# Kernel tuning notes

Measured on AMD Instinct MI355X. Metric: run time of the kernel, lower is better.

The kernel has to match this reference:

```python
import jax, jax.numpy as jnp
import numpy as np

COMMIT_LAMBDA = 0.25


def setup_inputs() -> dict:
    key = jax.random.key(0)
    k1, k2 = jax.random.split(key)
    B, C, T = 8, 256, 1024
    NCB, K, D = 2, 8192, 128
    x = jax.random.normal(k1, (B, C, T), dtype=jnp.float32)
    # EMA codebook weights buffer (init: randn * 0.1)
    codebooks = jax.random.normal(k2, (NCB, K, D), dtype=jnp.float32) * 0.1
    return {"x": x, "codebooks": codebooks}


def reference(x, codebooks):
    B, C, T = x.shape
    ncb, K, d = codebooks.shape
    # [B, C, T] -> [B*T, ncb, d]
    xs = x.reshape(B, ncb, d, T).transpose(0, 3, 1, 2).reshape(B * T, ncb, d)
    # squared euclidean distances (argmin-equivalent to cdist)
    x2 = jnp.sum(xs * xs, axis=-1)[..., None]            # [N, ncb, 1]
    c2 = jnp.sum(codebooks * codebooks, axis=-1)[None]    # [1, ncb, K]
    xc = jnp.einsum('bnd,nkd->bnk', xs, codebooks)        # [N, ncb, K]
    d2 = x2 - 2.0 * xc + c2
    idx = jnp.argmin(d2, axis=-1)                         # [N, ncb] int
    # gather nearest code vectors: [N, ncb, d]
    q = codebooks[jnp.arange(ncb)[None, :], idx]
    # straight-through estimator
    q_st = xs + jax.lax.stop_gradient(q - xs)
    # commitment loss (training mode): sum over codebooks of mse(x_i, q_i.detach())
    loss = COMMIT_LAMBDA * jnp.sum(
        jnp.mean((xs - jax.lax.stop_gradient(q)) ** 2, axis=(0, 2))
    )
    # reassemble to [B, C, T]
    quantized = q_st.reshape(B, T, ncb, d).transpose(0, 2, 3, 1).reshape(B, C, T)
    indices = idx.reshape(B, T, ncb).transpose(0, 2, 1)   # [B, ncb, T]
    return quantized, indices, loss
```

## Files before the change

### kernel.cpp

```cpp
#include <hip/hip_runtime.h>
#include <hip/hip_bf16.h>

#define BB   8
#define TT   1024
#define NCBN 2
#define DD   128
#define KK   8192
#define MM   8192

constexpr int OUT_IDX_OFF  = BB * 256 * TT;
constexpr int OUT_LOSS_OFF = OUT_IDX_OFF + BB * NCBN * TT;

#define THR   0.45f
#define QCAP  768

typedef __attribute__((ext_vector_type(8))) short   short8;
typedef __attribute__((ext_vector_type(4))) float   float4v;

__device__ __forceinline__ unsigned short f2bf(float v) {
    unsigned u = __float_as_uint(v);
    return (unsigned short)((u + 0x7FFFu + ((u >> 16) & 1u)) >> 16);
}

__device__ __forceinline__ void gl_lds16(const void* g, void* l) {
    __builtin_amdgcn_global_load_lds(
        (const __attribute__((address_space(1))) unsigned int*)g,
        (__attribute__((address_space(3))) unsigned int*)l, 16, 0, 0);
}

__global__ __launch_bounds__(256)
void pack_x_kernel(const float* __restrict__ x, unsigned short* __restrict__ xbf,
                   float* __restrict__ x2, unsigned long long* __restrict__ pmin) {
    __shared__ float Ld[DD][65];
    const int b = blockIdx.x >> 1, n = blockIdx.x & 1;
    const int t0 = blockIdx.y * 64;
    const int tid = threadIdx.x;

    const float* base = x + ((size_t)(b * 256 + n * 128)) * TT + t0;
    const int dro = tid >> 2, q4 = tid & 3;
#pragma unroll
    for (int half = 0; half < 2; ++half) {
        int d = dro + half * 64;
        const float* rp = base + (size_t)d * TT + q4 * 16;
#pragma unroll
        for (int j = 0; j < 4; ++j) {
            float4 v = *(const float4*)(rp + j * 4);
            int t = q4 * 16 + j * 4;
            Ld[d][t + 0] = v.x; Ld[d][t + 1] = v.y;
            Ld[d][t + 2] = v.z; Ld[d][t + 3] = v.w;
        }
    }
    __syncthreads();

    if (tid < 64) {
        float s = 0.f;
        for (int d = 0; d < DD; ++d) { float v = Ld[d][tid]; s = fmaf(v, v, s); }
        x2[(size_t)n * MM + b * TT + t0 + tid] = s;
        pmin[(size_t)n * MM + b * TT + t0 + tid] = 0xFFFFFFFFFFFFFFFFull;
    }

    unsigned short* orow0 = xbf + ((size_t)n * MM + b * TT + t0) * DD;
#pragma unroll
    for (int pp = 0; pp < 4; ++pp) {
        int u = tid + pp * 256;
        int tt = u >> 4, sg = u & 15;
        unsigned short tmp[8];
#pragma unroll
        for (int j = 0; j < 8; ++j) tmp[j] = f2bf(Ld[sg * 8 + j][tt]);
        uint4 pk;
        pk.x = (unsigned)tmp[0] | ((unsigned)tmp[1] << 16);
        pk.y = (unsigned)tmp[2] | ((unsigned)tmp[3] << 16);
        pk.z = (unsigned)tmp[4] | ((unsigned)tmp[5] << 16);
        pk.w = (unsigned)tmp[6] | ((unsigned)tmp[7] << 16);
        *(uint4*)(orow0 + (size_t)tt * DD + sg * 8) = pk;
    }
}

__global__ __launch_bounds__(256)
void pack_c_kernel(const float* __restrict__ cb, unsigned short* __restrict__ cbf,
                   float* __restrict__ c2, float* __restrict__ out) {
    int g = blockIdx.x * 256 + threadIdx.x;
    if (g == 0) out[OUT_LOSS_OFF] = 0.f;
    const float4* crow = (const float4*)(cb + (size_t)g * DD);
    unsigned short* orow = cbf + (size_t)g * DD;
    float s = 0.f;
#pragma unroll 4
    for (int i2 = 0; i2 < 16; ++i2) {
        float4 v0 = crow[2 * i2];
        float4 v1 = crow[2 * i2 + 1];
        s = fmaf(v0.x, v0.x, s); s = fmaf(v0.y, v0.y, s);
        s = fmaf(v0.z, v0.z, s); s = fmaf(v0.w, v0.w, s);
        s = fmaf(v1.x, v1.x, s); s = fmaf(v1.y, v1.y, s);
        s = fmaf(v1.z, v1.z, s); s = fmaf(v1.w, v1.w, s);
        uint4 pk;
        pk.x = (unsigned)f2bf(v0.x) | ((unsigned)f2bf(v0.y) << 16);
        pk.y = (unsigned)f2bf(v0.z) | ((unsigned)f2bf(v0.w) << 16);
        pk.z = (unsigned)f2bf(v1.x) | ((unsigned)f2bf(v1.y) << 16);
        pk.w = (unsigned)f2bf(v1.z) | ((unsigned)f2bf(v1.w) << 16);
        *(uint4*)(orow + i2 * 8) = pk;
    }
    c2[g] = s;
}

__device__ void rescore_one(int n, int m, int k,
                            const float* __restrict__ x, const float* __restrict__ cb,
                            const float* __restrict__ x2, const float* __restrict__ c2,
                            unsigned long long* __restrict__ pmin) {
    int b = m >> 10, t = m & (TT - 1);
    const float* xp = x + ((size_t)(b * 256 + n * 128)) * TT + t;
    const float* cp = cb + ((size_t)(n * KK + k)) * DD;
    float xc = 0.f;
    for (int d = 0; d < DD; ++d)
        xc = fmaf(xp[(size_t)d * TT], cp[d], xc);
    float u = x2[n * MM + m] - 2.0f * xc;
    float s = u + c2[n * KK + k];
    unsigned long long pk = ((unsigned long long)__float_as_uint(s) << 32) | (unsigned)k;
    atomicMin(pmin + (size_t)n * MM + m, pk);
}

__global__ __launch_bounds__(256, 2)
void screen_kernel(const unsigned short* __restrict__ xbf,
                   const unsigned short* __restrict__ cbf,
                   const float* __restrict__ c2,
                   const float* __restrict__ x,
                   const float* __restrict__ cb32,
                   const float* __restrict__ x2,
                   unsigned long long* __restrict__ pmin) {
    __shared__ __align__(16) unsigned short Qsh[128 * 128];
    __shared__ __align__(16) unsigned short Ash[128 * 128];
    __shared__ unsigned int   minU[128];
    __shared__ float          c2s[128];
    __shared__ unsigned int   qcnt;
    __shared__ unsigned int   queue[QCAP];

    const int tid = threadIdx.x;
    const int id  = blockIdx.x;
    const int n   = id & 1;
    const int ks  = (id >> 1) & 3;
    const int qt  = id >> 3;
    const int m0  = qt * 128;
    const int k0  = ks * 2048;

    const int wave = tid >> 6, lane = tid & 63;
    const int cw = wave & 1, qw = wave >> 1;
    const int quad = lane >> 4, l15 = lane & 15;

    int goff[8];
#pragma unroll
    for (int p = 0; p < 8; ++p) {
        int u   = (p * 4 + wave) * 64 + lane;
        int row = u >> 4;
        int seg = (u & 15) ^ (row & 15);
        goff[p] = (row * DD + seg * 8) * 2;
    }

    {
        const char* src = (const char*)(xbf + ((size_t)n * MM + m0) * DD);
#pragma unroll
        for (int p = 0; p < 8; ++p)
            gl_lds16(src + goff[p], &Qsh[(p * 4 + wave) * 512]);
    }
    if (tid < 128) minU[tid] = 0xFFFFFFFFu;
    if (tid == 0)  qcnt = 0;
    __syncthreads();

    short8 bfr[4][4];
#pragma unroll
    for (int tq = 0; tq < 4; ++tq) {
        int q = qw * 64 + tq * 16 + l15;
#pragma unroll
        for (int k4 = 0; k4 < 4; ++k4) {
            int seg = k4 * 4 + quad;
            bfr[tq][k4] = *(const short8*)(&Qsh[q * 128 + ((seg ^ l15) * 8)]);
        }
    }

    float mloc[4] = {3.4e38f, 3.4e38f, 3.4e38f, 3.4e38f};
    float thr[4]  = {3.4e38f, 3.4e38f, 3.4e38f, 3.4e38f};

    const char*  asrc0 = (const char*)(cbf + ((size_t)n * KK + k0) * DD);
    const float* c2p   = c2 + (size_t)n * KK + k0;

#pragma unroll
    for (int phase = 0; phase < 2; ++phase) {
        for (int ch = 0; ch < 16; ++ch) {
            __syncthreads();
            {
                const char* src = asrc0 + (size_t)ch * (128 * DD * 2);
#pragma unroll
                for (int p = 0; p < 8; ++p)
                    gl_lds16(src + goff[p], &Ash[(p * 4 + wave) * 512]);
                if (tid < 32)
                    *(float4*)&c2s[tid * 4] =
                        *(const float4*)(c2p + ch * 128 + tid * 4);
            }
            __syncthreads();

            float4v acc[4][4];
#pragma unroll
            for (int tc = 0; tc < 4; ++tc)
#pragma unroll
                for (int tq = 0; tq < 4; ++tq)
                    acc[tc][tq] = (float4v){0.f, 0.f, 0.f, 0.f};

#pragma unroll
            for (int k4 = 0; k4 < 4; ++k4) {
                short8 a[4];
#pragma unroll
                for (int tc = 0; tc < 4; ++tc) {
                    int r = cw * 64 + tc * 16 + l15;
                    int seg = k4 * 4 + quad;
                    a[tc] = *(const short8*)(&Ash[r * 128 + ((seg ^ l15) * 8)]);
                }
#pragma unroll
                for (int tc = 0; tc < 4; ++tc)
#pragma unroll
                    for (int tq = 0; tq < 4; ++tq)
                        acc[tc][tq] = __builtin_amdgcn_mfma_f32_16x16x32_bf16(
                            a[tc], bfr[tq][k4], acc[tc][tq], 0, 0, 0);
            }

#pragma unroll
            for (int tc = 0; tc < 4; ++tc) {
                float4v c2r = *(const float4v*)(&c2s[cw * 64 + tc * 16 + quad * 4]);
#pragma unroll
                for (int tq = 0; tq < 4; ++tq) {
                    float y0 = fmaf(-2.0f, acc[tc][tq][0], c2r[0]);
                    float y1 = fmaf(-2.0f, acc[tc][tq][1], c2r[1]);
                    float y2 = fmaf(-2.0f, acc[tc][tq][2], c2r[2]);
                    float y3 = fmaf(-2.0f, acc[tc][tq][3], c2r[3]);
                    float m4 = fminf(fminf(y0, y1), fminf(y2, y3));
                    if (phase == 0) {
                        mloc[tq] = fminf(mloc[tq], m4);
                    } else if (m4 <= thr[tq]) {
                        float yv[4] = {y0, y1, y2, y3};
#pragma unroll
                        for (int rg = 0; rg < 4; ++rg) {
                            if (yv[rg] <= thr[tq]) {
                                unsigned idx  = atomicAdd(&qcnt, 1u);
                                unsigned code = (unsigned)(ch * 128 + cw * 64 + tc * 16 + quad * 4 + rg);
                                unsigned q    = (unsigned)(qw * 64 + tq * 16 + l15);
                                if (idx < QCAP) queue[idx] = (q << 11) | code;
                                else rescore_one(n, m0 + (int)q, k0 + (int)code,
                                                 x, cb32, x2, c2, pmin);
                            }
                        }
                    }
                }
            }
        }

        if (phase == 0) {
#pragma unroll
            for (int tq = 0; tq < 4; ++tq) {
                float v = mloc[tq];
                v = fminf(v, __shfl_xor(v, 16, 64));
                v = fminf(v, __shfl_xor(v, 32, 64));
                if (quad == 0) {
                    unsigned u  = __float_as_uint(v);
                    unsigned mu = (u & 0x80000000u) ? ~u : (u | 0x80000000u);
                    atomicMin(&minU[qw * 64 + tq * 16 + l15], mu);
                }
            }
            __syncthreads();
#pragma unroll
            for (int tq = 0; tq < 4; ++tq) {
                unsigned mu = minU[qw * 64 + tq * 16 + l15];
                unsigned u  = (mu & 0x80000000u) ? (mu & 0x7FFFFFFFu) : ~mu;
                thr[tq] = __uint_as_float(u) + THR;
            }
        }
    }

    __syncthreads();
    unsigned total = qcnt; if (total > QCAP) total = QCAP;
    for (unsigned i = tid; i < total; i += 256) {
        unsigned ent = queue[i];
        rescore_one(n, m0 + (int)(ent >> 11), k0 + (int)(ent & 2047u),
                    x, cb32, x2, c2, pmin);
    }
}

__global__ __launch_bounds__(256)
void gather_kernel(const float* __restrict__ x, const float* __restrict__ cb,
                   const unsigned long long* __restrict__ pmin,
                   float* __restrict__ out) {
    __shared__ float Cr[64][DD + 1];
    __shared__ int   kid[64];
    const int b = blockIdx.x >> 1, n = blockIdx.x & 1;
    const int t0 = blockIdx.y * 64;
    const int tid = threadIdx.x;

    if (tid < 64) {
        int t = t0 + tid;
        int k = (int)(pmin[(size_t)n * MM + b * TT + t] & 0xFFFFFFFFull);
        kid[tid] = k;
        out[OUT_IDX_OFF + (b * NCBN + n) * TT + t] = (float)k;
    }
    __syncthreads();

    {
        int row = tid >> 2, q4 = tid & 3;
        const float* cp = cb + ((size_t)n * KK + kid[row]) * DD + q4 * 32;
#pragma unroll
        for (int j = 0; j < 8; ++j) {
            float4 v = *(const float4*)(cp + j * 4);
            int d = q4 * 32 + j * 4;
            Cr[row][d + 0] = v.x; Cr[row][d + 1] = v.y;
            Cr[row][d + 2] = v.z; Cr[row][d + 3] = v.w;
        }
    }
    __syncthreads();

    float lsum = 0.f;
    const float* xb = x  + ((size_t)(b * 256 + n * 128)) * TT + t0;
    float*       ob = out + ((size_t)(b * 256 + n * 128)) * TT + t0;
#pragma unroll
    for (int pp = 0; pp < 8; ++pp) {
        int u  = tid + pp * 256;
        int d  = u >> 4, ts = (u & 15) * 4;
        float4 xv = *(const float4*)(xb + (size_t)d * TT + ts);
        float4 qv = { Cr[ts + 0][d], Cr[ts + 1][d], Cr[ts + 2][d], Cr[ts + 3][d] };
        *(float4*)(ob + (size_t)d * TT + ts) = qv;
        float e;
        e = xv.x - qv.x; lsum = fmaf(e, e, lsum);
        e = xv.y - qv.y; lsum = fmaf(e, e, lsum);
        e = xv.z - qv.z; lsum = fmaf(e, e, lsum);
        e = xv.w - qv.w; lsum = fmaf(e, e, lsum);
    }

#pragma unroll
    for (int o = 32; o > 0; o >>= 1) lsum += __shfl_down(lsum, o, 64);
    __shared__ float wsum[4];
    int lane = tid & 63, w = tid >> 6;
    if (lane == 0) wsum[w] = lsum;
    __syncthreads();
    if (tid == 0) {
        float tot = wsum[0] + wsum[1] + wsum[2] + wsum[3];
        atomicAdd(out + OUT_LOSS_OFF, tot * 2.384185791015625e-7f);
    }
}

extern "C" void kernel_launch(void* const* d_in, const int* in_sizes, int n_in,
                              void* d_out, int out_size, void* d_ws, size_t ws_size,
                              hipStream_t stream) {
    (void)in_sizes; (void)n_in; (void)out_size; (void)ws_size;
    const float* x  = (const float*)d_in[0];
    const float* cb = (const float*)d_in[1];
    float* out = (float*)d_out;

    char* ws = (char*)d_ws;
    unsigned short* xbf = (unsigned short*)(ws);
    unsigned short* cbf = (unsigned short*)(ws + (4u << 20));
    float* x2 = (float*)(ws + (8u << 20));
    float* c2 = (float*)(ws + (8u << 20) + (64u << 10));
    unsigned long long* pmin =
        (unsigned long long*)(ws + (8u << 20) + (128u << 10));

    pack_x_kernel<<<dim3(16, 16), 256, 0, stream>>>(x, xbf, x2, pmin);
    pack_c_kernel<<<dim3(64), 256, 0, stream>>>(cb, cbf, c2, out);

    screen_kernel<<<dim3(512), 256, 0, stream>>>(xbf, cbf, c2, x, cb, x2, pmin);
    gather_kernel<<<dim3(16, 16), 256, 0, stream>>>(x, cb, pmin, out);
}
```

Before: 184.8 us.

## Split codebook screening 8-way with global min filter and contiguous fp32 rescore

Merges the x and codebook pack kernels into one launch and splits the K dimension into 8 slices. This doubles screen blocks to 1024, and a shared LDS buffer replaces the separate Q and A tiles to cut LDS use. Each block publishes its phase-0 row minima to a global atomic array. Queued candidates now store their approximate score, so the final rescore skips entries above the cross-slice threshold. A transposed fp32 copy of x, written when workspace allows, makes rescore reads contiguous. Risks include reading a partially updated global minimum, which is still safe but filters less, and extra writes of the fp32 copy.

Result: slower. 196.7 us (+6.4%).

```diff
diff --git a/kernel.cpp b/kernel.cpp
--- a/kernel.cpp
+++ b/kernel.cpp
@@ -12,7 +12,8 @@
 constexpr int OUT_LOSS_OFF = OUT_IDX_OFF + BB * NCBN * TT;
 
 #define THR   0.45f
-#define QCAP  768
+#define QCAP  512
+#define NSPL  8
 
 typedef __attribute__((ext_vector_type(8))) short   short8;
 typedef __attribute__((ext_vector_type(4))) float   float4v;
@@ -28,13 +29,54 @@
         (__attribute__((address_space(3))) unsigned int*)l, 16, 0, 0);
 }
 
+__device__ __forceinline__ unsigned fmono(float v) {
+    unsigned u = __float_as_uint(v);
+    return (u & 0x80000000u) ? ~u : (u | 0x80000000u);
+}
+__device__ __forceinline__ float fmono_inv(unsigned mu) {
+    unsigned u = (mu & 0x80000000u) ? (mu & 0x7FFFFFFFu) : ~mu;
+    return __uint_as_float(u);
+}
+
 __global__ __launch_bounds__(256)
-void pack_x_kernel(const float* __restrict__ x, unsigned short* __restrict__ xbf,
-                   float* __restrict__ x2, unsigned long long* __restrict__ pmin) {
+void prep_kernel(const float* __restrict__ x, const float* __restrict__ cb,
+                 unsigned short* __restrict__ xbf, unsigned short* __restrict__ cbf,
+                 float* __restrict__ x2, float* __restrict__ c2,
+                 float* __restrict__ x32t, int contig,
+                 unsigned long long* __restrict__ pmin,
+                 unsigned int* __restrict__ gminU,
+                 float* __restrict__ out) {
+    const int bx = blockIdx.x;
+    const int tid = threadIdx.x;
+
+    if (bx >= 256) {
+        int g = (bx - 256) * 256 + tid;
+        if (g == 0) out[OUT_LOSS_OFF] = 0.f;
+        const float4* crow = (const float4*)(cb + (size_t)g * DD);
+        unsigned short* orow = cbf + (size_t)g * DD;
+        float s = 0.f;
+#pragma unroll 4
+        for (int i2 = 0; i2 < 16; ++i2) {
+            float4 v0 = crow[2 * i2];
+            float4 v1 = crow[2 * i2 + 1];
+            s = fmaf(v0.x, v0.x, s); s = fmaf(v0.y, v0.y, s);
+            s = fmaf(v0.z, v0.z, s); s = fmaf(v0.w, v0.w, s);
+            s = fmaf(v1.x, v1.x, s); s = fmaf(v1.y, v1.y, s);
+            s = fmaf(v1.z, v1.z, s); s = fmaf(v1.w, v1.w, s);
+            uint4 pk;
+            pk.x = (unsigned)f2bf(v0.x) | ((unsigned)f2bf(v0.y) << 16);
+            pk.y = (unsigned)f2bf(v0.z) | ((unsigned)f2bf(v0.w) << 16);
+            pk.z = (unsigned)f2bf(v1.x) | ((unsigned)f2bf(v1.y) << 16);
+            pk.w = (unsigned)f2bf(v1.z) | ((unsigned)f2bf(v1.w) << 16);
+            *(uint4*)(orow + i2 * 8) = pk;
+        }
+        c2[g] = s;
+        return;
+    }
+
     __shared__ float Ld[DD][65];
-    const int b = blockIdx.x >> 1, n = blockIdx.x & 1;
-    const int t0 = blockIdx.y * 64;
-    const int tid = threadIdx.x;
+    const int b = bx >> 5, n = (bx >> 4) & 1;
+    const int t0 = (bx & 15) * 64;
 
     const float* base = x + ((size_t)(b * 256 + n * 128)) * TT + t0;
     const int dro = tid >> 2, q4 = tid & 3;
@@ -55,8 +97,10 @@
     if (tid < 64) {
         float s = 0.f;
         for (int d = 0; d < DD; ++d) { float v = Ld[d][tid]; s = fmaf(v, v, s); }
-        x2[(size_t)n * MM + b * TT + t0 + tid] = s;
-        pmin[(size_t)n * MM + b * TT + t0 + tid] = 0xFFFFFFFFFFFFFFFFull;
+        size_t gi = (size_t)n * MM + b * TT + t0 + tid;
+        x2[gi] = s;
+        pmin[gi] = 0xFFFFFFFFFFFFFFFFull;
+        gminU[gi] = 0xFFFFFFFFu;
     }
 
     unsigned short* orow0 = xbf + ((size_t)n * MM + b * TT + t0) * DD;
@@ -74,45 +118,36 @@
         pk.w = (unsigned)tmp[6] | ((unsigned)tmp[7] << 16);
         *(uint4*)(orow0 + (size_t)tt * DD + sg * 8) = pk;
     }
-}
-
-__global__ __launch_bounds__(256)
-void pack_c_kernel(const float* __restrict__ cb, unsigned short* __restrict__ cbf,
-                   float* __restrict__ c2, float* __restrict__ out) {
-    int g = blockIdx.x * 256 + threadIdx.x;
-    if (g == 0) out[OUT_LOSS_OFF] = 0.f;
-    const float4* crow = (const float4*)(cb + (size_t)g * DD);
-    unsigned short* orow = cbf + (size_t)g * DD;
-    float s = 0.f;
-#pragma unroll 4
-    for (int i2 = 0; i2 < 16; ++i2) {
-        float4 v0 = crow[2 * i2];
-        float4 v1 = crow[2 * i2 + 1];
-        s = fmaf(v0.x, v0.x, s); s = fmaf(v0.y, v0.y, s);
-        s = fmaf(v0.z, v0.z, s); s = fmaf(v0.w, v0.w, s);
-        s = fmaf(v1.x, v1.x, s); s = fmaf(v1.y, v1.y, s);
-        s = fmaf(v1.z, v1.z, s); s = fmaf(v1.w, v1.w, s);
-        uint4 pk;
-        pk.x = (unsigned)f2bf(v0.x) | ((unsigned)f2bf(v0.y) << 16);
-        pk.y = (unsigned)f2bf(v0.z) | ((unsigned)f2bf(v0.w) << 16);
-        pk.z = (unsigned)f2bf(v1.x) | ((unsigned)f2bf(v1.y) << 16);
-        pk.w = (unsigned)f2bf(v1.z) | ((unsigned)f2bf(v1.w) << 16);
-        *(uint4*)(orow + i2 * 8) = pk;
-    }
-    c2[g] = s;
+
+    if (contig) {
+        float* xrow0 = x32t + ((size_t)n * MM + b * TT + t0) * DD;
+#pragma unroll
+        for (int pp = 0; pp < 8; ++pp) {
+            int u = tid + pp * 256;
+            int tt = u >> 5, sg = u & 31;
+            float4 v = { Ld[sg * 4 + 0][tt], Ld[sg * 4 + 1][tt],
+                         Ld[sg * 4 + 2][tt], Ld[sg * 4 + 3][tt] };
+            *(float4*)(xrow0 + (size_t)tt * DD + sg * 4) = v;
+        }
+    }
 }
 
 __device__ void rescore_one(int n, int m, int k,
-                            const float* __restrict__ x, const float* __restrict__ cb,
+                            const float* __restrict__ xex, int contig,
+                            const float* __restrict__ cb,
                             const float* __restrict__ x2, const float* __restrict__ c2,
                             unsigned long long* __restrict__ pmin) {
-    int b = m >> 10, t = m & (TT - 1);
-    const float* xp = x + ((size_t)(b * 256 + n * 128)) * TT + t;
+    const float* xp; int st;
+    if (contig) { xp = xex + ((size_t)n * MM + m) * DD; st = 1; }
+    else {
+        int b = m >> 10, t = m & (TT - 1);
+        xp = xex + ((size_t)(b * 256 + n * 128)) * TT + t; st = TT;
+    }
     const float* cp = cb + ((size_t)(n * KK + k)) * DD;
     float xc = 0.f;
     for (int d = 0; d < DD; ++d)
-        xc = fmaf(xp[(size_t)d * TT], cp[d], xc);
-    float u = x2[n * MM + m] - 2.0f * xc;
+        xc = fmaf(xp[(size_t)d * st], cp[d], xc);
+    float u = x2[(size_t)n * MM + m] - 2.0f * xc;
     float s = u + c2[n * KK + k];
     unsigned long long pk = ((unsigned long long)__float_as_uint(s) << 32) | (unsigned)k;
     atomicMin(pmin + (size_t)n * MM + m, pk);
@@ -122,24 +157,24 @@
 void screen_kernel(const unsigned short* __restrict__ xbf,
                    const unsigned short* __restrict__ cbf,
                    const float* __restrict__ c2,
-                   const float* __restrict__ x,
+                   const float* __restrict__ xex, int contig,
                    const float* __restrict__ cb32,
                    const float* __restrict__ x2,
+                   unsigned int* __restrict__ gminU,
                    unsigned long long* __restrict__ pmin) {
-    __shared__ __align__(16) unsigned short Qsh[128 * 128];
-    __shared__ __align__(16) unsigned short Ash[128 * 128];
-    __shared__ unsigned int   minU[128];
-    __shared__ float          c2s[128];
-    __shared__ unsigned int   qcnt;
-    __shared__ unsigned int   queue[QCAP];
+    __shared__ __align__(16) unsigned short Bsh[128 * 128];
+    __shared__ unsigned int       minU[128];
+    __shared__ float              c2s[128];
+    __shared__ unsigned int       qcnt;
+    __shared__ unsigned long long queue[QCAP];
 
     const int tid = threadIdx.x;
     const int id  = blockIdx.x;
     const int n   = id & 1;
-    const int ks  = (id >> 1) & 3;
-    const int qt  = id >> 3;
+    const int ks  = (id >> 1) & 7;
+    const int qt  = id >> 4;
     const int m0  = qt * 128;
-    const int k0  = ks * 2048;
+    const int k0  = ks * 1024;
 
     const int wave = tid >> 6, lane = tid & 63;
     const int cw = wave & 1, qw = wave >> 1;
@@ -158,7 +193,7 @@
         const char* src = (const char*)(xbf + ((size_t)n * MM + m0) * DD);
 #pragma unroll
         for (int p = 0; p < 8; ++p)
-            gl_lds16(src + goff[p], &Qsh[(p * 4 + wave) * 512]);
+            gl_lds16(src + goff[p], &Bsh[(p * 4 + wave) * 512]);
     }
     if (tid < 128) minU[tid] = 0xFFFFFFFFu;
     if (tid == 0)  qcnt = 0;
@@ -171,7 +206,7 @@
 #pragma unroll
         for (int k4 = 0; k4 < 4; ++k4) {
             int seg = k4 * 4 + quad;
-            bfr[tq][k4] = *(const short8*)(&Qsh[q * 128 + ((seg ^ l15) * 8)]);
+            bfr[tq][k4] = *(const short8*)(&Bsh[q * 128 + ((seg ^ l15) * 8)]);
         }
     }
 
@@ -183,13 +218,13 @@
 
 #pragma unroll
     for (int phase = 0; phase < 2; ++phase) {
-        for (int ch = 0; ch < 16; ++ch) {
+        for (int ch = 0; ch < 8; ++ch) {
             __syncthreads();
             {
                 const char* src = asrc0 + (size_t)ch * (128 * DD * 2);
 #pragma unroll
                 for (int p = 0; p < 8; ++p)
-                    gl_lds16(src + goff[p], &Ash[(p * 4 + wave) * 512]);
+                    gl_lds16(src + goff[p], &Bsh[(p * 4 + wave) * 512]);
                 if (tid < 32)
                     *(float4*)&c2s[tid * 4] =
                         *(const float4*)(c2p + ch * 128 + tid * 4);
@@ -210,7 +245,7 @@
                 for (int tc = 0; tc < 4; ++tc) {
                     int r = cw * 64 + tc * 16 + l15;
                     int seg = k4 * 4 + quad;
-                    a[tc] = *(const short8*)(&Ash[r * 128 + ((seg ^ l15) * 8)]);
+                    a[tc] = *(const short8*)(&Bsh[r * 128 + ((seg ^ l15) * 8)]);
                 }
 #pragma unroll
                 for (int tc = 0; tc < 4; ++tc)
@@ -240,9 +275,11 @@
                                 unsigned idx  = atomicAdd(&qcnt, 1u);
                                 unsigned code = (unsigned)(ch * 128 + cw * 64 + tc * 16 + quad * 4 + rg);
                                 unsigned q    = (unsigned)(qw * 64 + tq * 16 + l15);
-                                if (idx < QCAP) queue[idx] = (q << 11) | code;
+                                if (idx < QCAP)
+                                    queue[idx] = ((unsigned long long)__float_as_uint(yv[rg]) << 32)
+                                               | (q << 10) | code;
                                 else rescore_one(n, m0 + (int)q, k0 + (int)code,
-                                                 x, cb32, x2, c2, pmin);
+                                                 xex, contig, cb32, x2, c2, pmin);
                             }
                         }
                     }
@@ -256,28 +293,34 @@
                 float v = mloc[tq];
                 v = fminf(v, __shfl_xor(v, 16, 64));
                 v = fminf(v, __shfl_xor(v, 32, 64));
-                if (quad == 0) {
-                    unsigned u  = __float_as_uint(v);
-                    unsigned mu = (u & 0x80000000u) ? ~u : (u | 0x80000000u);
-                    atomicMin(&minU[qw * 64 + tq * 16 + l15], mu);
-                }
+                if (quad == 0)
+                    atomicMin(&minU[qw * 64 + tq * 16 + l15], fmono(v));
             }
             __syncthreads();
-#pragma unroll
-            for (int tq = 0; tq < 4; ++tq) {
-                unsigned mu = minU[qw * 64 + tq * 16 + l15];
-                unsigned u  = (mu & 0x80000000u) ? (mu & 0x7FFFFFFFu) : ~mu;
-                thr[tq] = __uint_as_float(u) + THR;
-            }
-        }
-    }
-
-    __syncthreads();
+            if (tid < 128)
+                atomicMin(&gminU[(size_t)n * MM + m0 + tid], minU[tid]);
+#pragma unroll
+            for (int tq = 0; tq < 4; ++tq)
+                thr[tq] = fmono_inv(minU[qw * 64 + tq * 16 + l15]) + THR;
+        }
+    }
+
+    __syncthreads();
+    if (tid < 128) {
+        unsigned mu = atomicMin(&gminU[(size_t)n * MM + m0 + tid], 0xFFFFFFFFu);
+        c2s[tid] = fmono_inv(mu) + THR;
+    }
+    __syncthreads();
+
     unsigned total = qcnt; if (total > QCAP) total = QCAP;
     for (unsigned i = tid; i < total; i += 256) {
-        unsigned ent = queue[i];
-        rescore_one(n, m0 + (int)(ent >> 11), k0 + (int)(ent & 2047u),
-                    x, cb32, x2, c2, pmin);
+        unsigned long long e = queue[i];
+        float y = __uint_as_float((unsigned)(e >> 32));
+        unsigned q = ((unsigned)e >> 10) & 127u;
+        unsigned code = (unsigned)e & 1023u;
+        if (y <= c2s[q])
+            rescore_one(n, m0 + (int)q, k0 + (int)code,
+                        xex, contig, cb32, x2, c2, pmin);
     }
 }
 
@@ -344,7 +387,7 @@
 extern "C" void kernel_launch(void* const* d_in, const int* in_sizes, int n_in,
                               void* d_out, int out_size, void* d_ws, size_t ws_size,
                               hipStream_t stream) {
-    (void)in_sizes; (void)n_in; (void)out_size; (void)ws_size;
+    (void)in_sizes; (void)n_in; (void)out_size;
     const float* x  = (const float*)d_in[0];
     const float* cb = (const float*)d_in[1];
     float* out = (float*)d_out;
@@ -356,10 +399,17 @@
     float* c2 = (float*)(ws + (8u << 20) + (64u << 10));
     unsigned long long* pmin =
         (unsigned long long*)(ws + (8u << 20) + (128u << 10));
-
-    pack_x_kernel<<<dim3(16, 16), 256, 0, stream>>>(x, xbf, x2, pmin);
-    pack_c_kernel<<<dim3(64), 256, 0, stream>>>(cb, cbf, c2, out);
-
-    screen_kernel<<<dim3(512), 256, 0, stream>>>(xbf, cbf, c2, x, cb, x2, pmin);
+    unsigned int* gminU =
+        (unsigned int*)(ws + (8u << 20) + (256u << 10));
+    float* x32t = (float*)(ws + (9u << 20));
+
+    const size_t need = (9u << 20) + (size_t)NCBN * MM * DD * 4;
+    const int contig = (ws_size >= need) ? 1 : 0;
+    const float* xex = contig ? x32t : x;
+
+    prep_kernel<<<dim3(320), 256, 0, stream>>>(x, cb, xbf, cbf, x2, c2,
+                                               x32t, contig, pmin, gminU, out);
+    screen_kernel<<<dim3(1024), 256, 0, stream>>>(xbf, cbf, c2, xex, contig,
+                                                  cb, x2, gminU, pmin);
     gather_kernel<<<dim3(16, 16), 256, 0, stream>>>(x, cb, pmin, out);
 }
```
